# Kernel tuning notes

Measured on AMD Instinct MI355X. Metric: run time of the kernel, lower is better.

The kernel has to match this reference:

```python
import itertools
import jax, jax.numpy as jnp
import numpy as np

B = 1024      # graphs
N = 40        # atoms per graph (module supports 1..49)
ETA = 64
K = 32        # num_clusters
ZD = 32       # z_dim
NA = 10       # num_atom_types
NB = 5        # num_bond_types + 1
CH, AH, BH = 128, 128, 64
TAU = 1.0


def _resblock(x, W1, b1, W2, b2, Ws, bs):
    # assumed ResidualBlock: Linear->ReLU->(dropout, eval=identity)->Linear + linear skip
    h = jax.nn.relu(x @ W1 + b1)
    return h @ W2 + b2 + (x @ Ws + bs)


def setup_inputs() -> dict:
    key = jax.random.key(0)
    ks = jax.random.split(key, 24)
    s = 0.05
    pairs = np.array(list(itertools.combinations(range(N), 2)), dtype=np.int32)  # [780,2]
    offsets = (np.arange(B, dtype=np.int32) * N)[:, None, None]
    edge_index = jnp.asarray((pairs[None] + offsets).reshape(-1, 2))  # [B*780, 2]
    return {
        "eta": jax.random.normal(ks[0], (B, ETA), jnp.float32),
        "gumbel_noise": jax.random.gumbel(ks[1], (B * N, K), jnp.float32),
        "z_noise": jax.random.normal(ks[2], (B * N, ZD), jnp.float32),
        "cW1": jax.random.normal(ks[3], (ETA, CH)) * s, "cb1": jnp.zeros((CH,)),
        "cW2": jax.random.normal(ks[4], (CH, K)) * s, "cb2": jnp.zeros((K,)),
        "cWs": jax.random.normal(ks[5], (ETA, K)) * s, "cbs": jnp.zeros((K,)),
        "cluster_means": jax.random.normal(ks[6], (K, ZD)),
        "cluster_log_sigmas": jnp.full((K, ZD), -2.0),
        "aW1": jax.random.normal(ks[7], (ZD, AH)) * s, "ab1": jnp.zeros((AH,)),
        "aW2": jax.random.normal(ks[8], (AH, NA)) * s, "ab2": jnp.zeros((NA,)),
        "aWs": jax.random.normal(ks[9], (ZD, NA)) * s, "abs_": jnp.zeros((NA,)),
        "bond_matrix": jax.random.normal(ks[10], (NB, ZD, ZD)),
        "bW1": jax.random.normal(ks[11], (NB, BH)) * s, "bb1": jnp.zeros((BH,)),
        "bW2": jax.random.normal(ks[12], (BH, NB)) * s, "bb2": jnp.zeros((NB,)),
        "bWs": jax.random.normal(ks[13], (NB, NB)) * s, "bbs": jnp.zeros((NB,)),
        "edge_index": edge_index,
    }


def reference(eta, gumbel_noise, z_noise,
              cW1, cb1, cW2, cb2, cWs, cbs,
              cluster_means, cluster_log_sigmas,
              aW1, ab1, aW2, ab2, aWs, abs_,
              bond_matrix, bW1, bb1, bW2, bb2, bWs, bbs,
              edge_index):
    # decode_eta: mixture weights
    pi = jax.nn.softmax(_resblock(eta, cW1, cb1, cW2, cb2, cWs, cbs), axis=1)  # [B,K]
    log_pi = jnp.log(pi)
    # sample_c: gumbel-softmax (hard, straight-through) per node
    logits = jnp.repeat(log_pi, N, axis=0)                      # [B*N, K]
    y_soft = jax.nn.softmax((logits + gumbel_noise) / TAU, axis=-1)
    y_hard = jax.nn.one_hot(jnp.argmax(y_soft, axis=-1), K, dtype=y_soft.dtype)
    c = y_hard + y_soft - jax.lax.stop_gradient(y_soft)         # straight-through
    # sample_z
    mu = c @ cluster_means                                      # [B*N, ZD]
    log_sigma = c @ cluster_log_sigmas
    sigma = jnp.exp(jnp.clip(log_sigma, -20.0, 30.0))
    z = z_noise * sigma + mu
    # decode_z: atom logits
    atom_types = _resblock(z, aW1, ab1, aW2, ab2, aWs, abs_)    # [B*N, NA]
    # symmetrized per-bond-type bilinear form over edge node pairs
    Wsym = 0.5 * (bond_matrix + jnp.swapaxes(bond_matrix, 1, 2))  # [NB, ZD, ZD]
    zi = z[edge_index[:, 0]]                                    # [E, ZD]
    zj = z[edge_index[:, 1]]                                    # [E, ZD]
    bil = jnp.einsum('ed,tdc,ec->et', zi, Wsym, zj)             # [E, NB]
    edge_logits = _resblock(bil, bW1, bb1, bW2, bb2, bWs, bbs)
    edge_types = jax.nn.softmax(edge_logits, axis=1)            # [E, NB]
    return atom_types, edge_types
```

## Files before the change

### kernel.cpp

```cpp
#include <hip/hip_runtime.h>

constexpr int NPAIR = 780;

constexpr int OFF_ZT = 0;
constexpr int OFF_A  = 1280;
constexpr int UTP    = 1280;
constexpr int OFF_BT = 5120;
constexpr int SH_TOT = 9020;

__global__ __launch_bounds__(256) void prep_kernel(
    const float* __restrict__ eta,
    const float* __restrict__ cW1, const float* __restrict__ cb1,
    const float* __restrict__ cW2, const float* __restrict__ cb2,
    const float* __restrict__ cWs, const float* __restrict__ cbs,
    const float* __restrict__ bond, const float* __restrict__ lsig,
    const float* __restrict__ bW1, const float* __restrict__ bb1,
    const float* __restrict__ bW2, const float* __restrict__ bb2,
    const float* __restrict__ bWs, const float* __restrict__ bbs,
    float* __restrict__ log_pi, float* __restrict__ wsym,
    float* __restrict__ sigma, float* __restrict__ hwg)
{
  if (blockIdx.x < 256) {
    const int lane = threadIdx.x & 63, wid = threadIdx.x >> 6;
    const int row = blockIdx.x * 4 + wid;
    __shared__ __align__(16) float etas[4][64];
    __shared__ __align__(16) float hs[4][128];
    etas[wid][lane] = eta[row * 64 + lane];
    __syncthreads();
    float a0 = cb1[lane], a1 = cb1[lane + 64];
    for (int d = 0; d < 64; ++d) {
      float ed = etas[wid][d];
      a0 += ed * cW1[d * 128 + lane];
      a1 += ed * cW1[d * 128 + lane + 64];
    }
    hs[wid][lane] = fmaxf(a0, 0.f);
    hs[wid][lane + 64] = fmaxf(a1, 0.f);
    __syncthreads();
    if (lane < 32) {
      float x = cb2[lane] + cbs[lane];
      for (int j = 0; j < 128; ++j) x += hs[wid][j] * cW2[j * 32 + lane];
      for (int d = 0; d < 64; ++d) x += etas[wid][d] * cWs[d * 32 + lane];
      float m = x;
      for (int off = 16; off; off >>= 1) m = fmaxf(m, __shfl_xor(m, off));
      float e = __expf(x - m);
      float s = e;
      for (int off = 16; off; off >>= 1) s += __shfl_xor(s, off);
      log_pi[row * 32 + lane] = (x - m) - __logf(s);
    }
  } else {
    const int e = (blockIdx.x - 256) * 256 + threadIdx.x;
    if (e < 5120) {
      const int t = e >> 10, r = e & 1023, c = r >> 5, d = r & 31;
      wsym[e] = 0.5f * (bond[e] + bond[t * 1024 + d * 32 + c]);
    } else if (e < 6144) {
      const int q = e - 5120;
      sigma[q] = __expf(fminf(fmaxf(lsig[q], -20.f), 30.f));
    } else if (e < 6888) {
      const int idx = e - 6144;
      float v;
      if (idx < 320) v = bW1[idx];
      else if (idx < 384) v = bb1[idx - 320];
      else if (idx < 704) { int qq = idx - 384; int t2 = qq >> 6, j = qq & 63; v = bW2[j * 5 + t2]; }
      else if (idx < 709) v = bb2[idx - 704];
      else if (idx < 734) v = bWs[idx - 709];
      else v = bbs[idx - 734];
      hwg[idx] = v;
    }
  }
}

__global__ __launch_bounds__(256, 4) void fused_kernel(
    const float* __restrict__ log_pi, const float* __restrict__ gumbel,
    const float* __restrict__ z_noise,
    const float* __restrict__ means, const float* __restrict__ sigma,
    const float* __restrict__ aW1, const float* __restrict__ ab1,
    const float* __restrict__ aW2, const float* __restrict__ ab2,
    const float* __restrict__ aWs, const float* __restrict__ abs_,
    const float* __restrict__ wsym, const float* __restrict__ hwg,
    float* __restrict__ atom_out, float* __restrict__ edge_out)
{
  __shared__ __align__(16) float S[SH_TOT];
  const int tid = threadIdx.x;
  const int m = blockIdx.x;

  if (tid < 40) {
    const int n = m * 40 + tid;
    float lp[32];
    #pragma unroll
    for (int c = 0; c < 32; ++c) lp[c] = log_pi[m * 32 + c];
    float g[32];
    const float4* g4 = (const float4*)(gumbel + (size_t)n * 32);
    #pragma unroll
    for (int q = 0; q < 8; ++q) {
      float4 v = g4[q];
      g[4*q] = v.x; g[4*q+1] = v.y; g[4*q+2] = v.z; g[4*q+3] = v.w;
    }
    int kb = 0; float vb = lp[0] + g[0];
    #pragma unroll
    for (int c = 1; c < 32; ++c) {
      float v = lp[c] + g[c];
      if (v > vb) { vb = v; kb = c; }
    }
    const float4* zn4 = (const float4*)(z_noise + (size_t)n * 32);
    const float4* mk4 = (const float4*)(means + kb * 32);
    const float4* sg4 = (const float4*)(sigma + kb * 32);
    #pragma unroll
    for (int q = 0; q < 8; ++q) {
      float4 zn = zn4[q], mk = mk4[q], sg = sg4[q];
      S[OFF_ZT + (4*q    ) * 40 + tid] = zn.x * sg.x + mk.x;
      S[OFF_ZT + (4*q + 1) * 40 + tid] = zn.y * sg.y + mk.y;
      S[OFF_ZT + (4*q + 2) * 40 + tid] = zn.z * sg.z + mk.z;
      S[OFF_ZT + (4*q + 3) * 40 + tid] = zn.w * sg.w + mk.w;
    }
  }
  __syncthreads();

  for (int u = tid; u < 320; u += 256) {
    const int ng = u >> 5, jg = u & 31;
    const int n0 = ng * 4, j0 = jg * 4;
    float acc[4][4];
    #pragma unroll
    for (int a = 0; a < 4; ++a)
      #pragma unroll
      for (int b = 0; b < 4; ++b) acc[a][b] = 0.f;
    #pragma unroll 8
    for (int c = 0; c < 32; ++c) {
      float4 zv = *(const float4*)&S[OFF_ZT + c * 40 + n0];
      float4 wv = *(const float4*)(aW1 + c * 128 + j0);
      acc[0][0] += zv.x * wv.x; acc[0][1] += zv.x * wv.y; acc[0][2] += zv.x * wv.z; acc[0][3] += zv.x * wv.w;
      acc[1][0] += zv.y * wv.x; acc[1][1] += zv.y * wv.y; acc[1][2] += zv.y * wv.z; acc[1][3] += zv.y * wv.w;
      acc[2][0] += zv.z * wv.x; acc[2][1] += zv.z * wv.y; acc[2][2] += zv.z * wv.z; acc[2][3] += zv.z * wv.w;
      acc[3][0] += zv.w * wv.x; acc[3][1] += zv.w * wv.y; acc[3][2] += zv.w * wv.z; acc[3][3] += zv.w * wv.w;
    }
    float4 bv = *(const float4*)(ab1 + j0);
    #pragma unroll
    for (int a = 0; a < 4; ++a) {
      float4 hv;
      hv.x = fmaxf(acc[a][0] + bv.x, 0.f);
      hv.y = fmaxf(acc[a][1] + bv.y, 0.f);
      hv.z = fmaxf(acc[a][2] + bv.z, 0.f);
      hv.w = fmaxf(acc[a][3] + bv.w, 0.f);
      *(float4*)&S[OFF_A + (n0 + a) * 132 + j0] = hv;
    }
  }
  __syncthreads();

  if (tid < 200) {
    const int n = tid / 5, kp = tid - (tid / 5) * 5, k0 = kp * 2;
    float a0 = ab2[k0] + abs_[k0];
    float a1 = ab2[k0 + 1] + abs_[k0 + 1];
    #pragma unroll 8
    for (int c = 0; c < 32; ++c) {
      float zc = S[OFF_ZT + c * 40 + n];
      float2 w = *(const float2*)(aWs + c * 10 + k0);
      a0 += zc * w.x; a1 += zc * w.y;
    }
    #pragma unroll 8
    for (int j = 0; j < 128; ++j) {
      float hv = S[OFF_A + n * 132 + j];
      float2 w = *(const float2*)(aW2 + j * 10 + k0);
      a0 += hv * w.x; a1 += hv * w.y;
    }
    *(float2*)(atom_out + (size_t)m * 400 + n * 10 + k0) = make_float2(a0, a1);
  }
  __syncthreads();

  #pragma unroll
  for (int R = 0; R < 2; ++R) {
    const int tbase = (R == 0) ? 0 : 3;
    const int nplanes = (R == 0) ? 3 : 2;
    if (tid < nplanes * 80) {
      const int tl = tid / 80, r = tid - tl * 80;
      const int dg = r / 10, ig = r - dg * 10;
      const int d0 = dg * 4, i0 = ig * 4;
      const float* wg = wsym + (tbase + tl) * 1024;
      float acc[4][4];
      #pragma unroll
      for (int a = 0; a < 4; ++a)
        #pragma unroll
        for (int b = 0; b < 4; ++b) acc[a][b] = 0.f;
      #pragma unroll 8
      for (int c = 0; c < 32; ++c) {
        float4 zv = *(const float4*)&S[OFF_ZT + c * 40 + i0];
        float4 wv = *(const float4*)(wg + c * 32 + d0);
        acc[0][0] += wv.x * zv.x; acc[0][1] += wv.x * zv.y; acc[0][2] += wv.x * zv.z; acc[0][3] += wv.x * zv.w;
        acc[1][0] += wv.y * zv.x; acc[1][1] += wv.y * zv.y; acc[1][2] += wv.y * zv.z; acc[1][3] += wv.y * zv.w;
        acc[2][0] += wv.z * zv.x; acc[2][1] += wv.z * zv.y; acc[2][2] += wv.z * zv.z; acc[2][3] += wv.z * zv.w;
        acc[3][0] += wv.w * zv.x; acc[3][1] += wv.w * zv.y; acc[3][2] += wv.w * zv.z; acc[3][3] += wv.w * zv.w;
      }
      #pragma unroll
      for (int a = 0; a < 4; ++a)
        *(float4*)&S[OFF_A + tl * UTP + (d0 + a) * 40 + i0] =
            make_float4(acc[a][0], acc[a][1], acc[a][2], acc[a][3]);
    }
    __syncthreads();

    if (tid < nplanes * 55) {
      const int tl = tid / 55;
      int q = tid - tl * 55;
      int ig = 0;
      while (q >= 10 - ig) { q -= 10 - ig; ++ig; }
      const int jg = ig + q;
      const int i0 = ig * 4, j0 = jg * 4;
      float acc[4][4];
      #pragma unroll
      for (int a = 0; a < 4; ++a)
        #pragma unroll
        for (int b = 0; b < 4; ++b) acc[a][b] = 0.f;
      #pragma unroll 8
      for (int d = 0; d < 32; ++d) {
        float4 uv = *(const float4*)&S[OFF_A + tl * UTP + d * 40 + i0];
        float4 zv = *(const float4*)&S[OFF_ZT + d * 40 + j0];
        acc[0][0] += uv.x * zv.x; acc[0][1] += uv.x * zv.y; acc[0][2] += uv.x * zv.z; acc[0][3] += uv.x * zv.w;
        acc[1][0] += uv.y * zv.x; acc[1][1] += uv.y * zv.y; acc[1][2] += uv.y * zv.z; acc[1][3] += uv.y * zv.w;
        acc[2][0] += uv.z * zv.x; acc[2][1] += uv.z * zv.y; acc[2][2] += uv.z * zv.z; acc[2][3] += uv.z * zv.w;
        acc[3][0] += uv.w * zv.x; acc[3][1] += uv.w * zv.y; acc[3][2] += uv.w * zv.z; acc[3][3] += uv.w * zv.w;
      }
      const int tg = tbase + tl;
      #pragma unroll
      for (int a = 0; a < 4; ++a) {
        const int i = i0 + a;
        #pragma unroll
        for (int b = 0; b < 4; ++b) {
          const int j = j0 + b;
          if (i < j) {
            const int p = i * (79 - i) / 2 + (j - i - 1);
            S[OFF_BT + tg * 780 + p] = acc[a][b];
          }
        }
      }
    }
    __syncthreads();
  }

  const float* w1h = hwg;
  const float* b1h = hwg + 320;
  const float* w2t = hwg + 384;
  const float* b2h = hwg + 704;
  const float* wsh = hwg + 709;
  const float* bsh = hwg + 734;

  float bil5[3][5], lg[3][5];
  #pragma unroll
  for (int s = 0; s < 3; ++s) {
    const int p = tid + (s << 8);
    #pragma unroll
    for (int t = 0; t < 5; ++t) bil5[s][t] = S[OFF_BT + t * 780 + p];
    #pragma unroll
    for (int t2 = 0; t2 < 5; ++t2) {
      float a = b2h[t2] + bsh[t2];
      #pragma unroll
      for (int t = 0; t < 5; ++t) a += bil5[s][t] * wsh[t * 5 + t2];
      lg[s][t2] = a;
    }
  }
  for (int j4 = 0; j4 < 16; ++j4) {
    float4 bb = ((const float4*)b1h)[j4];
    float4 h[3];
    #pragma unroll
    for (int s = 0; s < 3; ++s) h[s] = bb;
    #pragma unroll
    for (int t = 0; t < 5; ++t) {
      float4 w1 = ((const float4*)(w1h + t * 64))[j4];
      #pragma unroll
      for (int s = 0; s < 3; ++s) {
        float bt = bil5[s][t];
        h[s].x += bt * w1.x; h[s].y += bt * w1.y; h[s].z += bt * w1.z; h[s].w += bt * w1.w;
      }
    }
    #pragma unroll
    for (int s = 0; s < 3; ++s) {
      h[s].x = fmaxf(h[s].x, 0.f); h[s].y = fmaxf(h[s].y, 0.f);
      h[s].z = fmaxf(h[s].z, 0.f); h[s].w = fmaxf(h[s].w, 0.f);
    }
    #pragma unroll
    for (int t2 = 0; t2 < 5; ++t2) {
      float4 w2 = ((const float4*)(w2t + t2 * 64))[j4];
      #pragma unroll
      for (int s = 0; s < 3; ++s)
        lg[s][t2] += h[s].x * w2.x + h[s].y * w2.y + h[s].z * w2.z + h[s].w * w2.w;
    }
  }
  #pragma unroll
  for (int s = 0; s < 3; ++s) {
    const int p = tid + (s << 8);
    float mx = lg[s][0];
    #pragma unroll
    for (int t2 = 1; t2 < 5; ++t2) mx = fmaxf(mx, lg[s][t2]);
    float e[5], sum = 0.f;
    #pragma unroll
    for (int t2 = 0; t2 < 5; ++t2) { e[t2] = __expf(lg[s][t2] - mx); sum += e[t2]; }
    float inv = 1.f / sum;
    float* outp = edge_out + ((size_t)m * NPAIR + p) * 5;
    #pragma unroll
    for (int t2 = 0; t2 < 5; ++t2) outp[t2] = e[t2] * inv;
  }

  if (tid < 12) {
    const int p = 768 + tid;
    float bt[5], lgt[5];
    #pragma unroll
    for (int t = 0; t < 5; ++t) bt[t] = S[OFF_BT + t * 780 + p];
    #pragma unroll
    for (int t2 = 0; t2 < 5; ++t2) {
      float a = b2h[t2] + bsh[t2];
      #pragma unroll
      for (int t = 0; t < 5; ++t) a += bt[t] * wsh[t * 5 + t2];
      lgt[t2] = a;
    }
    for (int j = 0; j < 64; ++j) {
      float hv = b1h[j];
      #pragma unroll
      for (int t = 0; t < 5; ++t) hv += bt[t] * w1h[t * 64 + j];
      hv = fmaxf(hv, 0.f);
      #pragma unroll
      for (int t2 = 0; t2 < 5; ++t2) lgt[t2] += hv * w2t[t2 * 64 + j];
    }
    float mx = lgt[0];
    #pragma unroll
    for (int t2 = 1; t2 < 5; ++t2) mx = fmaxf(mx, lgt[t2]);
    float e[5], sum = 0.f;
    #pragma unroll
    for (int t2 = 0; t2 < 5; ++t2) { e[t2] = __expf(lgt[t2] - mx); sum += e[t2]; }
    float inv = 1.f / sum;
    float* outp = edge_out + ((size_t)m * NPAIR + p) * 5;
    #pragma unroll
    for (int t2 = 0; t2 < 5; ++t2) outp[t2] = e[t2] * inv;
  }
}

extern "C" void kernel_launch(void* const* d_in, const int* in_sizes, int n_in,
                              void* d_out, int out_size, void* d_ws, size_t ws_size,
                              hipStream_t stream) {
  const float* eta    = (const float*)d_in[0];
  const float* gumbel = (const float*)d_in[1];
  const float* z_noise= (const float*)d_in[2];
  const float* cW1 = (const float*)d_in[3];
  const float* cb1 = (const float*)d_in[4];
  const float* cW2 = (const float*)d_in[5];
  const float* cb2 = (const float*)d_in[6];
  const float* cWs = (const float*)d_in[7];
  const float* cbs = (const float*)d_in[8];
  const float* means = (const float*)d_in[9];
  const float* lsig  = (const float*)d_in[10];
  const float* aW1 = (const float*)d_in[11];
  const float* ab1 = (const float*)d_in[12];
  const float* aW2 = (const float*)d_in[13];
  const float* ab2 = (const float*)d_in[14];
  const float* aWs = (const float*)d_in[15];
  const float* abs_= (const float*)d_in[16];
  const float* bond= (const float*)d_in[17];
  const float* bW1 = (const float*)d_in[18];
  const float* bb1 = (const float*)d_in[19];
  const float* bW2 = (const float*)d_in[20];
  const float* bb2 = (const float*)d_in[21];
  const float* bWs = (const float*)d_in[22];
  const float* bbs = (const float*)d_in[23];

  float* wsym   = (float*)d_ws;
  float* sigma  = wsym + 5120;
  float* hwg    = sigma + 1024;
  float* log_pi = hwg + 768;
  float* atom_out = (float*)d_out;
  float* edge_out = atom_out + (size_t)1024 * 400;

  prep_kernel<<<284, 256, 0, stream>>>(eta, cW1, cb1, cW2, cb2, cWs, cbs,
                                       bond, lsig, bW1, bb1, bW2, bb2, bWs, bbs,
                                       log_pi, wsym, sigma, hwg);
  fused_kernel<<<1024, 256, 0, stream>>>(log_pi, gumbel, z_noise,
                                         means, sigma, aW1, ab1, aW2, ab2, aWs, abs_,
                                         wsym, hwg, atom_out, edge_out);
}
```

Measured before the change: 181.8 us.

## Rebalance per-wave work and merge bond-plane passes into a single shared-memory phase

The cluster argmax is split across four lanes per atom with shuffle reduction, instead of 40 threads each scanning all 32 clusters. Atom-hidden, U-projection and bilinear work units are spread evenly across all four waves. All five bond planes are now computed in one pass rather than two rounds of 3+2. Bilinear results are held in registers across a barrier so the bond-logit buffer can alias the U scratch area, which shrinks shared memory and removes a round of barriers. The cost is more registers per thread, which may limit occupancy.

```diff
diff --git a/kernel.cpp b/kernel.cpp
--- a/kernel.cpp
+++ b/kernel.cpp
@@ -5,8 +5,8 @@
 constexpr int OFF_ZT = 0;
 constexpr int OFF_A  = 1280;
 constexpr int UTP    = 1280;
-constexpr int OFF_BT = 5120;
-constexpr int SH_TOT = 9020;
+constexpr int OFF_BT = 1280;
+constexpr int SH_TOT = 7680;
 
 __global__ __launch_bounds__(256) void prep_kernel(
     const float* __restrict__ eta,
@@ -81,72 +81,86 @@
 {
   __shared__ __align__(16) float S[SH_TOT];
   const int tid = threadIdx.x;
+  const int lane = tid & 63, wid = tid >> 6;
   const int m = blockIdx.x;
 
-  if (tid < 40) {
-    const int n = m * 40 + tid;
-    float lp[32];
-    #pragma unroll
-    for (int c = 0; c < 32; ++c) lp[c] = log_pi[m * 32 + c];
-    float g[32];
-    const float4* g4 = (const float4*)(gumbel + (size_t)n * 32);
-    #pragma unroll
-    for (int q = 0; q < 8; ++q) {
-      float4 v = g4[q];
-      g[4*q] = v.x; g[4*q+1] = v.y; g[4*q+2] = v.z; g[4*q+3] = v.w;
-    }
-    int kb = 0; float vb = lp[0] + g[0];
-    #pragma unroll
-    for (int c = 1; c < 32; ++c) {
-      float v = lp[c] + g[c];
-      if (v > vb) { vb = v; kb = c; }
-    }
-    const float4* zn4 = (const float4*)(z_noise + (size_t)n * 32);
-    const float4* mk4 = (const float4*)(means + kb * 32);
-    const float4* sg4 = (const float4*)(sigma + kb * 32);
-    #pragma unroll
-    for (int q = 0; q < 8; ++q) {
+  if (lane < 40) {
+    const int n = wid * 10 + (lane >> 2);
+    const int sub = lane & 3;
+    const int c0 = sub * 8;
+    const int n_glb = m * 40 + n;
+    const float4* lp4 = (const float4*)(log_pi + m * 32 + c0);
+    const float4* g4  = (const float4*)(gumbel + (size_t)n_glb * 32 + c0);
+    float vals[8];
+    {
+      float4 a = lp4[0], b = g4[0];
+      vals[0] = a.x + b.x; vals[1] = a.y + b.y; vals[2] = a.z + b.z; vals[3] = a.w + b.w;
+    }
+    {
+      float4 a = lp4[1], b = g4[1];
+      vals[4] = a.x + b.x; vals[5] = a.y + b.y; vals[6] = a.z + b.z; vals[7] = a.w + b.w;
+    }
+    int kb = c0; float vb = vals[0];
+    #pragma unroll
+    for (int q = 1; q < 8; ++q)
+      if (vals[q] > vb) { vb = vals[q]; kb = c0 + q; }
+    #pragma unroll
+    for (int off = 1; off <= 2; off <<= 1) {
+      float vo = __shfl_xor(vb, off);
+      int   ko = __shfl_xor(kb, off);
+      if (vo > vb || (vo == vb && ko < kb)) { vb = vo; kb = ko; }
+    }
+    const float4* zn4 = (const float4*)(z_noise + (size_t)n_glb * 32 + c0);
+    const float4* mk4 = (const float4*)(means + kb * 32 + c0);
+    const float4* sg4 = (const float4*)(sigma + kb * 32 + c0);
+    #pragma unroll
+    for (int q = 0; q < 2; ++q) {
       float4 zn = zn4[q], mk = mk4[q], sg = sg4[q];
-      S[OFF_ZT + (4*q    ) * 40 + tid] = zn.x * sg.x + mk.x;
-      S[OFF_ZT + (4*q + 1) * 40 + tid] = zn.y * sg.y + mk.y;
-      S[OFF_ZT + (4*q + 2) * 40 + tid] = zn.z * sg.z + mk.z;
-      S[OFF_ZT + (4*q + 3) * 40 + tid] = zn.w * sg.w + mk.w;
+      const int r = c0 + 4 * q;
+      S[OFF_ZT + (r    ) * 40 + n] = zn.x * sg.x + mk.x;
+      S[OFF_ZT + (r + 1) * 40 + n] = zn.y * sg.y + mk.y;
+      S[OFF_ZT + (r + 2) * 40 + n] = zn.z * sg.z + mk.z;
+      S[OFF_ZT + (r + 3) * 40 + n] = zn.w * sg.w + mk.w;
     }
   }
   __syncthreads();
 
-  for (int u = tid; u < 320; u += 256) {
-    const int ng = u >> 5, jg = u & 31;
-    const int n0 = ng * 4, j0 = jg * 4;
-    float acc[4][4];
-    #pragma unroll
-    for (int a = 0; a < 4; ++a)
-      #pragma unroll
-      for (int b = 0; b < 4; ++b) acc[a][b] = 0.f;
-    #pragma unroll 8
-    for (int c = 0; c < 32; ++c) {
-      float4 zv = *(const float4*)&S[OFF_ZT + c * 40 + n0];
-      float4 wv = *(const float4*)(aW1 + c * 128 + j0);
-      acc[0][0] += zv.x * wv.x; acc[0][1] += zv.x * wv.y; acc[0][2] += zv.x * wv.z; acc[0][3] += zv.x * wv.w;
-      acc[1][0] += zv.y * wv.x; acc[1][1] += zv.y * wv.y; acc[1][2] += zv.y * wv.z; acc[1][3] += zv.y * wv.w;
-      acc[2][0] += zv.z * wv.x; acc[2][1] += zv.z * wv.y; acc[2][2] += zv.z * wv.z; acc[2][3] += zv.z * wv.w;
-      acc[3][0] += zv.w * wv.x; acc[3][1] += zv.w * wv.y; acc[3][2] += zv.w * wv.z; acc[3][3] += zv.w * wv.w;
-    }
-    float4 bv = *(const float4*)(ab1 + j0);
-    #pragma unroll
-    for (int a = 0; a < 4; ++a) {
-      float4 hv;
-      hv.x = fmaxf(acc[a][0] + bv.x, 0.f);
-      hv.y = fmaxf(acc[a][1] + bv.y, 0.f);
-      hv.z = fmaxf(acc[a][2] + bv.z, 0.f);
-      hv.w = fmaxf(acc[a][3] + bv.w, 0.f);
-      *(float4*)&S[OFF_A + (n0 + a) * 132 + j0] = hv;
-    }
+  {
+    auto atomh = [&](int u) {
+      const int n0 = (u >> 5) * 4, j0 = (u & 31) * 4;
+      float acc[4][4];
+      #pragma unroll
+      for (int a = 0; a < 4; ++a)
+        #pragma unroll
+        for (int b = 0; b < 4; ++b) acc[a][b] = 0.f;
+      #pragma unroll 8
+      for (int c = 0; c < 32; ++c) {
+        float4 zv = *(const float4*)&S[OFF_ZT + c * 40 + n0];
+        float4 wv = *(const float4*)(aW1 + c * 128 + j0);
+        acc[0][0] += zv.x * wv.x; acc[0][1] += zv.x * wv.y; acc[0][2] += zv.x * wv.z; acc[0][3] += zv.x * wv.w;
+        acc[1][0] += zv.y * wv.x; acc[1][1] += zv.y * wv.y; acc[1][2] += zv.y * wv.z; acc[1][3] += zv.y * wv.w;
+        acc[2][0] += zv.z * wv.x; acc[2][1] += zv.z * wv.y; acc[2][2] += zv.z * wv.z; acc[2][3] += zv.z * wv.w;
+        acc[3][0] += zv.w * wv.x; acc[3][1] += zv.w * wv.y; acc[3][2] += zv.w * wv.z; acc[3][3] += zv.w * wv.w;
+      }
+      float4 bv = *(const float4*)(ab1 + j0);
+      #pragma unroll
+      for (int a = 0; a < 4; ++a) {
+        float4 hv;
+        hv.x = fmaxf(acc[a][0] + bv.x, 0.f);
+        hv.y = fmaxf(acc[a][1] + bv.y, 0.f);
+        hv.z = fmaxf(acc[a][2] + bv.z, 0.f);
+        hv.w = fmaxf(acc[a][3] + bv.w, 0.f);
+        *(float4*)&S[OFF_A + (n0 + a) * 132 + j0] = hv;
+      }
+    };
+    atomh(wid * 80 + lane);
+    if (lane < 16) atomh(wid * 80 + 64 + lane);
   }
   __syncthreads();
 
-  if (tid < 200) {
-    const int n = tid / 5, kp = tid - (tid / 5) * 5, k0 = kp * 2;
+  if (lane < 50) {
+    const int idx = wid * 50 + lane;
+    const int n = idx / 5, kp = idx - n * 5, k0 = kp * 2;
     float a0 = ab2[k0] + abs_[k0];
     float a1 = ab2[k0 + 1] + abs_[k0 + 1];
     #pragma unroll 8
@@ -165,15 +179,13 @@
   }
   __syncthreads();
 
-  #pragma unroll
-  for (int R = 0; R < 2; ++R) {
-    const int tbase = (R == 0) ? 0 : 3;
-    const int nplanes = (R == 0) ? 3 : 2;
-    if (tid < nplanes * 80) {
-      const int tl = tid / 80, r = tid - tl * 80;
+  {
+    auto uunit = [&](int u) {
+      const int tl = u / 80;
+      const int r = u - tl * 80;
       const int dg = r / 10, ig = r - dg * 10;
       const int d0 = dg * 4, i0 = ig * 4;
-      const float* wg = wsym + (tbase + tl) * 1024;
+      const float* wg = wsym + tl * 1024;
       float acc[4][4];
       #pragma unroll
       for (int a = 0; a < 4; ++a)
@@ -192,17 +204,21 @@
       for (int a = 0; a < 4; ++a)
         *(float4*)&S[OFF_A + tl * UTP + (d0 + a) * 40 + i0] =
             make_float4(acc[a][0], acc[a][1], acc[a][2], acc[a][3]);
-    }
-    __syncthreads();
-
-    if (tid < nplanes * 55) {
-      const int tl = tid / 55;
-      int q = tid - tl * 55;
+    };
+    uunit(wid * 100 + lane);
+    if (lane < 36) uunit(wid * 100 + 64 + lane);
+  }
+  __syncthreads();
+
+  {
+    auto bdecode = [&](int u, int& tl, int& i0, int& j0) {
+      tl = u / 55;
+      int q = u - tl * 55;
       int ig = 0;
       while (q >= 10 - ig) { q -= 10 - ig; ++ig; }
-      const int jg = ig + q;
-      const int i0 = ig * 4, j0 = jg * 4;
-      float acc[4][4];
+      i0 = ig * 4; j0 = (ig + q) * 4;
+    };
+    auto bcompute = [&](int tl, int i0, int j0, float (&acc)[4][4]) {
       #pragma unroll
       for (int a = 0; a < 4; ++a)
         #pragma unroll
@@ -216,7 +232,8 @@
         acc[2][0] += uv.z * zv.x; acc[2][1] += uv.z * zv.y; acc[2][2] += uv.z * zv.z; acc[2][3] += uv.z * zv.w;
         acc[3][0] += uv.w * zv.x; acc[3][1] += uv.w * zv.y; acc[3][2] += uv.w * zv.z; acc[3][3] += uv.w * zv.w;
       }
-      const int tg = tbase + tl;
+    };
+    auto bscatter = [&](int tl, int i0, int j0, float (&acc)[4][4]) {
       #pragma unroll
       for (int a = 0; a < 4; ++a) {
         const int i = i0 + a;
@@ -225,13 +242,26 @@
           const int j = j0 + b;
           if (i < j) {
             const int p = i * (79 - i) / 2 + (j - i - 1);
-            S[OFF_BT + tg * 780 + p] = acc[a][b];
+            S[OFF_BT + tl * 780 + p] = acc[a][b];
           }
         }
       }
-    }
+    };
+    const int u1 = wid * 69 + lane;
+    int tl1, i01, j01;
+    bdecode(u1, tl1, i01, j01);
+    float acc1[4][4];
+    bcompute(tl1, i01, j01, acc1);
+    const int u2 = wid * 69 + 64 + lane;
+    const bool has2 = (lane < 5) && (u2 < 275);
+    int tl2 = 0, i02 = 0, j02 = 0;
+    float acc2[4][4];
+    if (has2) { bdecode(u2, tl2, i02, j02); bcompute(tl2, i02, j02, acc2); }
     __syncthreads();
-  }
+    bscatter(tl1, i01, j01, acc1);
+    if (has2) bscatter(tl2, i02, j02, acc2);
+  }
+  __syncthreads();
 
   const float* w1h = hwg;
   const float* b1h = hwg + 320;
```

New measurement: 187.9 us. 1.03x slower.
